# Optimization experiments

Measured on AMD Instinct MI355X. Metric: run time of the kernel, lower is better.

The kernel has to match this reference:

```python
import jax, jax.numpy as jnp
import numpy as np

B, N, NFEAT = 8, 5000, 15
NUM_CLASSES_IN = 12          # len(elem_labels)
D_IN = NUM_CLASSES_IN + NFEAT - 1  # 26
D_DIST = 256
D_HID = 256
BIN_SIZE = 100
NBINS = N // BIN_SIZE        # 50
K = 16                       # num_neighbors
DIST_MULT = 0.1
MAX_HALF_BINS = 100          # max_num_bins // 2
NUM_ID_OUT, NUM_REG_OUT = 8, 4


def _pairwise_dist(A):
    # A: [nbins, bs, d] -> [nbins, bs, bs]
    na = jnp.sum(A * A, -1)
    d2 = na[..., :, None] - 2.0 * jnp.einsum('...nd,...md->...nm', A, A) + na[..., None, :]
    return jnp.sqrt(jnp.maximum(d2, 1e-6))


def _build_edges(points, rot):
    # points: [N, D_DIST]; LSH binning then per-bin kNN (exp(-dist_mult * dist) affinities)
    mul = points @ rot[:, :NBINS // 2]
    cmul = jnp.concatenate([mul, -mul], axis=-1)
    bin_idx = jnp.argmax(cmul, axis=-1)
    bins_split = jnp.argsort(bin_idx).reshape(NBINS, BIN_SIZE)   # [nbins, bs] point ids
    parts = points[bins_split]                                   # [nbins, bs, d]
    dm = jnp.exp(-DIST_MULT * _pairwise_dist(parts))             # [nbins, bs, bs]
    vals, idx = jax.lax.top_k(dm, K)                             # [nbins, bs, K]
    dst = jax.vmap(lambda b, i: b[i])(bins_split, idx)           # global dst ids
    src = jnp.broadcast_to(bins_split[:, :, None], dst.shape)
    return src.reshape(-1), dst.reshape(-1), vals.reshape(-1)    # nnz = N*K


def _ghconv(x, src, dst, vals, theta, W_h, W_t, b_t):
    # x: [N, H]; edge list (src, dst, vals); duplicates sum, matching tf.sparse.add
    deg = jax.ops.segment_sum(vals, src, num_segments=N)
    norm = jnp.power(deg + 1e-6, -0.5)[:, None]
    f_hom = (x @ theta) * norm
    agg = jax.ops.segment_sum(vals[:, None] * f_hom[dst], src, num_segments=N) * norm
    f_het = x @ W_h
    gate = jax.nn.sigmoid(x @ W_t + b_t)
    return jax.nn.selu(gate * agg + (1.0 - gate) * f_het)


def setup_inputs() -> dict:
    key = jax.random.key(0)
    ks = jax.random.split(key, 32)
    w = lambda i, shape, s=0.02: (s * jax.random.normal(ks[i], shape)).astype(jnp.float32)
    ids = jax.random.randint(ks[0], (B, N, 1), 0, NUM_CLASSES_IN).astype(jnp.float32)
    props = jax.random.normal(ks[1], (B, N, NFEAT - 1), dtype=jnp.float32)
    X = jnp.concatenate([ids, props], axis=-1)
    return {
        'X': X,
        'rot': w(2, (D_DIST, MAX_HALF_BINS), 1.0),
        'W_emb': w(3, (D_IN, D_DIST)), 'b_emb': w(4, (D_DIST,)),
        'Wenc_id': w(5, (D_IN, D_HID)), 'benc_id': w(6, (D_HID,)),
        'theta_id': w(7, (D_HID, D_HID)), 'Wh_id': w(8, (D_HID, D_HID)),
        'Wt_id': w(9, (D_HID, D_HID)), 'bt_id': w(10, (D_HID,)),
        'Wdec_id': w(11, (D_HID, D_HID)), 'bdec_id': w(12, (D_HID,)),
        'Wout_id': w(13, (D_HID, NUM_ID_OUT)), 'bout_id': w(14, (NUM_ID_OUT,)),
        'Wenc_reg': w(15, (D_IN, D_HID)), 'benc_reg': w(16, (D_HID,)),
        'theta_reg': w(17, (D_HID, D_HID)), 'Wh_reg': w(18, (D_HID, D_HID)),
        'Wt_reg': w(19, (D_HID, D_HID)), 'bt_reg': w(20, (D_HID,)),
        'Wdec_reg': w(21, (D_HID, D_HID)), 'bdec_reg': w(22, (D_HID,)),
        'Wout_reg': w(23, (D_HID, NUM_REG_OUT)), 'bout_reg': w(24, (NUM_REG_OUT,)),
    }


def reference(X, rot, W_emb, b_emb,
              Wenc_id, benc_id, theta_id, Wh_id, Wt_id, bt_id, Wdec_id, bdec_id, Wout_id, bout_id,
              Wenc_reg, benc_reg, theta_reg, Wh_reg, Wt_reg, bt_reg, Wdec_reg, bdec_reg, Wout_reg, bout_reg):
    # InputEncoding: one-hot class id + remaining features
    enc = jnp.concatenate(
        [jax.nn.one_hot(X[:, :, 0].astype(jnp.int32), NUM_CLASSES_IN, dtype=jnp.float32),
         X[:, :, 1:]], axis=-1)                                  # [B, N, 26]
    emb = enc @ W_emb + b_emb                                     # distance embedding
    src, dst, vals = jax.vmap(_build_edges, in_axes=(0, None))(emb, rot)

    def branch(Wenc, benc, theta, Wh, Wt, bt, Wdec, bdec, Wout, bout):
        x = jax.nn.selu(enc @ Wenc + benc)
        x = jax.vmap(lambda xb, s, d, v: _ghconv(xb, s, d, v, theta, Wh, Wt, bt))(x, src, dst, vals)
        x = jax.nn.selu(x @ Wdec + bdec)
        return x @ Wout + bout

    out_id = branch(Wenc_id, benc_id, theta_id, Wh_id, Wt_id, bt_id, Wdec_id, bdec_id, Wout_id, bout_id)
    out_reg = branch(Wenc_reg, benc_reg, theta_reg, Wh_reg, Wt_reg, bt_reg, Wdec_reg, bdec_reg, Wout_reg, bout_reg)
    return out_id, out_reg
```

## Files before the change

### kernel.cpp

```cpp
#include <hip/hip_runtime.h>
#include <hip/hip_bf16.h>
#include <cstdint>
#include <cstddef>

#define NB     8
#define NLOC   5000
#define NPTS   40000
#define DIN    26
#define DH     256
#define NBINS  50
#define BSZ    100
#define KNN    16
#define KP     104

static const size_t OFF_BHI  = 40960000;
static const size_t OFF_BLO  = 41353216;
static const size_t OFF_BDHI = 41746432;
static const size_t OFF_BDLO = 41877504;
static const size_t OFF_ENC  = 81920000;
static const size_t OFF_BIN  = 86080000;
static const size_t OFF_ORD  = 86240000;
static const size_t OFF_NRM  = 86400000;
static const size_t OFF_EVAL = 86560000;
static const size_t OFF_EDST = 89120000;
static const size_t OFF_KEYS = 91680000;
static const size_t OFF_AXHI = 91680000;
static const size_t OFF_AXLO = 112160000;
static const size_t OFF_NA   = 132640000;
static const size_t OFF_FHET = 132640000;
static const size_t OFF_GATE = 173600000;

typedef __attribute__((ext_vector_type(8))) short short8;
typedef __attribute__((ext_vector_type(4))) float f32x4;

__device__ __forceinline__ float selu_f(float x) {
  const float scale = 1.0507009873554805f, alpha = 1.6732632423543772f;
  return x > 0.f ? scale * x : scale * alpha * expm1f(x);
}

__device__ __forceinline__ void split_bf16(float v, __hip_bfloat16& h, __hip_bfloat16& l) {
  h = __float2bfloat16(v);
  l = __float2bfloat16(v - __bfloat162float(h));
}

#define EPB 16
__global__ __launch_bounds__(256) void k_enc_emb(
    const float* __restrict__ X, const float* __restrict__ Wemb,
    const float* __restrict__ bemb, float* __restrict__ enc,
    double* __restrict__ emb) {
  __shared__ float xb[EPB * 15];
  const int tid = threadIdx.x;
  const int r0 = blockIdx.x * EPB;
  if (tid < EPB * 15) xb[tid] = X[(size_t)r0 * 15 + tid];
  double wcol[DIN];
  #pragma unroll
  for (int c = 0; c < DIN; c++) wcol[c] = (double)Wemb[c * DH + tid];
  const double bcol = (double)bemb[tid];
  __syncthreads();
  #pragma unroll 1
  for (int p = 0; p < EPB; p++) {
    const int id = (int)xb[p * 15];
    double acc = 0.0;
    #pragma unroll
    for (int c = 0; c < 12; c++)
      acc += ((c == id) ? 1.0 : 0.0) * wcol[c];
    #pragma unroll
    for (int c = 12; c < DIN; c++)
      acc += (double)xb[p * 15 + (c - 11)] * wcol[c];
    emb[(size_t)(r0 + p) * DH + tid] = acc + bcol;
  }
  #pragma unroll
  for (int t = 0; t < 2; t++) {
    int idx = t * 256 + tid;
    if (idx < EPB * DIN) {
      int p = idx / DIN, c = idx - p * DIN;
      int id = (int)xb[p * 15];
      float v = (c < 12) ? ((c == id) ? 1.f : 0.f) : xb[p * 15 + (c - 11)];
      enc[(size_t)(r0 + p) * DIN + c] = v;
    }
  }
}

#define MULPTS 16
__global__ __launch_bounds__(512) void k_mul(
    const double* __restrict__ emb, const float* __restrict__ rot,
    int* __restrict__ bin_idx) {
  __shared__ double ebuf[MULPTS][258];
  __shared__ float  rotT[25][257];
  __shared__ double mulb[MULPTS][26];
  const int tid = threadIdx.x;
  const int r0 = blockIdx.x * MULPTS;
  for (int idx = tid; idx < 25 * DH; idx += 512) {
    int d = idx / 25, j = idx - d * 25;
    rotT[j][d] = rot[d * 100 + j];
  }
  for (int idx = tid; idx < MULPTS * DH; idx += 512) {
    int p = idx >> 8, d = idx & 255;
    ebuf[p][d] = emb[(size_t)(r0 + p) * DH + d];
  }
  __syncthreads();
  if (tid < MULPTS * 25) {
    int p = tid / 25, j = tid - p * 25;
    double a = 0.0;
    #pragma unroll 4
    for (int d = 0; d < DH; d++) a += ebuf[p][d] * (double)rotT[j][d];
    mulb[p][j] = a;
  }
  __syncthreads();
  if (tid < MULPTS) {
    double best = -1e300; int bi = 0;
    #pragma unroll 1
    for (int jj = 0; jj < 2 * 25; jj++) {
      double v = (jj < 25) ? mulb[tid][jj] : -mulb[tid][jj - 25];
      if (v > best) { best = v; bi = jj; }
    }
    bin_idx[r0 + tid] = bi;
  }
}

#define SCH 20
__global__ __launch_bounds__(256) void k_sort(
    const int* __restrict__ bin_idx, int* __restrict__ order) {
  const int b = blockIdx.x;
  __shared__ unsigned short cnt[256][NBINS + 2];
  __shared__ int base[NBINS];
  __shared__ int bl[NLOC];
  const int tid = threadIdx.x;
  for (int j = 0; j < NBINS; j++) cnt[tid][j] = 0;
  for (int n = tid; n < NLOC; n += 256) bl[n] = bin_idx[b * NLOC + n];
  __syncthreads();
  const int s = tid * SCH;
  const int e = (s + SCH < NLOC) ? s + SCH : NLOC;
  for (int n = s; n < e; n++) cnt[tid][bl[n]]++;
  __syncthreads();
  if (tid < NBINS) {
    int run = 0;
    for (int t = 0; t < 256; t++) {
      int c = cnt[t][tid];
      cnt[t][tid] = (unsigned short)run;
      run += c;
    }
    base[tid] = run;
  }
  __syncthreads();
  if (tid == 0) {
    int r = 0;
    for (int j = 0; j < NBINS; j++) { int t = base[j]; base[j] = r; r += t; }
  }
  __syncthreads();
  for (int n = s; n < e; n++) {
    int j = bl[n];
    int pos = base[j] + cnt[tid][j];
    cnt[tid][j]++;
    order[b * NLOC + pos] = n;
  }
}

__global__ __launch_bounds__(256) void k_norm(
    const double* __restrict__ emb, const int* __restrict__ order,
    double* __restrict__ na) {
  const int s = blockIdx.x * 4 + (threadIdx.x >> 6);
  const int lane = threadIdx.x & 63;
  const int row = (s / NLOC) * NLOC + order[s];
  const double* p = &emb[(size_t)row * DH + lane * 4];
  double2 a = *(const double2*)p;
  double2 b = *(const double2*)(p + 2);
  double sum = a.x * a.x + a.y * a.y + b.x * b.x + b.y * b.y;
  #pragma unroll
  for (int off = 32; off >= 1; off >>= 1) sum += __shfl_xor(sum, off);
  if (lane == 0) na[s] = sum;
}

#define DQR 112
__global__ __launch_bounds__(256) void k_dist(
    const double* __restrict__ emb, const int* __restrict__ order,
    const double* __restrict__ na, double* __restrict__ keys) {
  __shared__ double P[DQR][34];
  __shared__ double naL[DQR];
  __shared__ int rid[DQR];
  const int bin = blockIdx.x;
  const int rh  = blockIdx.y;
  const int gb0 = bin * BSZ;
  const int brow = (bin / NBINS) * NLOC;
  const int tid = threadIdx.x;
  const int tx = tid & 15, ty = tid >> 4;
  if (tid < DQR) {
    int rr = tid < BSZ ? tid : BSZ - 1;
    rid[tid] = brow + order[gb0 + rr];
    naL[tid] = na[gb0 + rr];
  }
  __syncthreads();
  size_t srow[7];
  int scol[7], sr[7];
  #pragma unroll
  for (int q = 0; q < 7; q++) {
    int idx = q * 256 + tid;
    sr[q] = idx >> 4;
    scol[q] = (idx & 15) * 2;
    srow[q] = (size_t)rid[sr[q]] * DH;
  }
  int ar[4];
  #pragma unroll
  for (int i = 0; i < 4; i++) {
    int pr = rh * 50 + ty + 16 * i;
    ar[i] = pr < DQR ? pr : DQR - 1;
  }
  double acc[4][7] = {};
  double2 buf[7];
  #pragma unroll
  for (int q = 0; q < 7; q++)
    buf[q] = *(const double2*)&emb[srow[q] + scol[q]];
  for (int kc = 0; kc < 8; kc++) {
    __syncthreads();
    #pragma unroll
    for (int q = 0; q < 7; q++) {
      P[sr[q]][scol[q]]     = buf[q].x;
      P[sr[q]][scol[q] + 1] = buf[q].y;
    }
    __syncthreads();
    if (kc < 7) {
      #pragma unroll
      for (int q = 0; q < 7; q++)
        buf[q] = *(const double2*)&emb[srow[q] + (kc + 1) * 32 + scol[q]];
    }
    #pragma unroll 2
    for (int kk = 0; kk < 32; kk++) {
      double b[7];
      #pragma unroll
      for (int j = 0; j < 7; j++) b[j] = P[tx + 16 * j][kk];
      #pragma unroll
      for (int i = 0; i < 4; i++) {
        double a = P[ar[i]][kk];
        #pragma unroll
        for (int j = 0; j < 7; j++) acc[i][j] += a * b[j];
      }
    }
  }
  #pragma unroll
  for (int i = 0; i < 4; i++) {
    int lr = ty + 16 * i;
    if (lr >= 50) continue;
    int gi = rh * 50 + lr;
    #pragma unroll
    for (int j = 0; j < 7; j++) {
      int gj = tx + 16 * j;
      if (gj >= BSZ) continue;
      double t = naL[gi] - 2.0 * acc[i][j];
      t += naL[gj];
      keys[(size_t)(gb0 + gi) * KP + gj] = (t > 1e-6) ? t : 1e-6;
    }
  }
}

__global__ __launch_bounds__(256) void k_topk(
    const double* __restrict__ keys, float* __restrict__ evals,
    int* __restrict__ edstl, float* __restrict__ normv) {
  const int g = threadIdx.x >> 4;
  const int l = threadIdx.x & 15;
  const int row = blockIdx.x * 16 + g;
  const unsigned long long* kr =
      (const unsigned long long*)(keys + (size_t)row * KP);
  unsigned long long c[7];
  #pragma unroll
  for (int s = 0; s < 7; s++) {
    int j = s * 16 + l;
    c[s] = (j < BSZ) ? kr[j] : ~0ull;
  }
  float deg = 0.f, myev = 0.f;
  int myidx = 0;
  #pragma unroll 1
  for (int k = 0; k < KNN; k++) {
    unsigned long long mv = c[0];
    int ms = 0;
    #pragma unroll
    for (int s = 1; s < 7; s++)
      if (c[s] < mv) { mv = c[s]; ms = s; }
    int idx = ms * 16 + l;
    #pragma unroll
    for (int off = 8; off >= 1; off >>= 1) {
      unsigned long long ov = __shfl_xor(mv, off);
      int oi = __shfl_xor(idx, off);
      if (ov < mv || (ov == mv && oi < idx)) { mv = ov; idx = oi; }
    }
    float ev = expf(-0.1f * sqrtf((float)__longlong_as_double(mv)));
    deg += ev;
    if (l == k) { myev = ev; myidx = idx; }
    const int own = idx & 15, slot = idx >> 4;
    if (l == own) {
      #pragma unroll
      for (int s = 0; s < 7; s++)
        if (slot == s) c[s] = ~0ull;
    }
  }
  evals[(size_t)row * KNN + l] = myev;
  edstl[(size_t)row * KNN + l] = myidx;
  if (l == 0) normv[row] = 1.f / sqrtf(deg + 1e-6f);
}

__global__ __launch_bounds__(256) void k_encmm(
    const float* __restrict__ enc, const float* __restrict__ W,
    const float* __restrict__ bias, __hip_bfloat16* __restrict__ hi,
    __hip_bfloat16* __restrict__ lo) {
  const int r = blockIdx.x;
  __shared__ float e[DIN];
  const int tid = threadIdx.x;
  if (tid < DIN) e[tid] = enc[(size_t)r * DIN + tid];
  __syncthreads();
  float acc = 0.f;
  #pragma unroll 1
  for (int c = 0; c < DIN; c++) acc += e[c] * W[c * DH + tid];
  float v = selu_f(acc + bias[tid]);
  __hip_bfloat16 h, l;
  split_bf16(v, h, l);
  hi[(size_t)r * DH + tid] = h;
  lo[(size_t)r * DH + tid] = l;
}

__global__ __launch_bounds__(256) void k_cvt_w4(
    const float* __restrict__ W0, const float* __restrict__ W1,
    const float* __restrict__ W2, const float* __restrict__ W3,
    __hip_bfloat16* __restrict__ Bhi, __hip_bfloat16* __restrict__ Blo,
    __hip_bfloat16* __restrict__ Bdhi, __hip_bfloat16* __restrict__ Bdlo) {
  __shared__ float t[32][33];
  const int z = blockIdx.z;
  const float* W = (z == 0) ? W0 : (z == 1) ? W1 : (z == 2) ? W2 : W3;
  __hip_bfloat16* hi = (z < 3) ? Bhi + (size_t)z * 65536 : Bdhi;
  __hip_bfloat16* lo = (z < 3) ? Blo + (size_t)z * 65536 : Bdlo;
  const int tid = threadIdx.x, tx = tid & 31, ty = tid >> 5;
  const int k0 = blockIdx.x * 32, n0 = blockIdx.y * 32;
  #pragma unroll
  for (int r = 0; r < 4; r++)
    t[ty + r * 8][tx] = W[(size_t)(k0 + ty + r * 8) * 256 + n0 + tx];
  __syncthreads();
  #pragma unroll
  for (int r = 0; r < 4; r++) {
    int n = ty + r * 8;
    float v = t[tx][n];
    __hip_bfloat16 h, l;
    split_bf16(v, h, l);
    hi[(size_t)(n0 + n) * 256 + k0 + tx] = h;
    lo[(size_t)(n0 + n) * 256 + k0 + tx] = l;
  }
}

#define MF_SMEM (4 * 128 * 40 * 2)
template <int MODE>
__global__ __launch_bounds__(256, 4) void k_mfma(
    const ushort* __restrict__ Ahi, const ushort* __restrict__ Alo,
    const ushort* __restrict__ Bhi, const ushort* __restrict__ Blo,
    const float* __restrict__ bias,
    float* __restrict__ O0, float* __restrict__ O1, float* __restrict__ O2) {
  extern __shared__ char mfs[];
  short* As0 = (short*)mfs;
  short* As1 = As0 + 128 * 40;
  short* Bs0 = As1 + 128 * 40;
  short* Bs1 = Bs0 + 128 * 40;
  const int NX = (MODE == 0) ? 6 : 2;
  const int total = NX * 313;
  const int q = total >> 3, rr8 = total & 7;
  const int xcd = blockIdx.x & 7, pos = blockIdx.x >> 3;
  const int lw = (xcd < rr8 ? xcd * (q + 1) : rr8 * (q + 1) + (xcd - rr8) * q) + pos;
  const int m0 = (lw / NX) * 128;
  const int nx = lw - (lw / NX) * NX;
  const int n0 = nx * 128;
  const int tid = threadIdx.x;
  const int lane = tid & 63, wid = tid >> 6;
  const int wr = wid >> 1, wc = wid & 1;
  const int lm = lane & 15, lg = lane >> 4;
  f32x4 acc[4][4];
  #pragma unroll
  for (int i = 0; i < 4; i++)
    #pragma unroll
    for (int j = 0; j < 4; j++)
      #pragma unroll
      for (int r = 0; r < 4; r++) acc[i][j][r] = 0.f;

  for (int k0 = 0; k0 < 256; k0 += 32) {
    #pragma unroll
    for (int it = 0; it < 2; it++) {
      int idx = it * 256 + tid;
      int r = idx >> 2, c = (idx & 3) * 8;
      int gm = m0 + r; if (gm >= NPTS) gm = NPTS - 1;
      *(uint4*)&As0[r * 40 + c] = *(const uint4*)&Ahi[(size_t)gm * 256 + k0 + c];
      *(uint4*)&As1[r * 40 + c] = *(const uint4*)&Alo[(size_t)gm * 256 + k0 + c];
      *(uint4*)&Bs0[r * 40 + c] = *(const uint4*)&Bhi[(size_t)(n0 + r) * 256 + k0 + c];
      *(uint4*)&Bs1[r * 40 + c] = *(const uint4*)&Blo[(size_t)(n0 + r) * 256 + k0 + c];
    }
    __syncthreads();
    const int lk = lg * 8;
    short8 aH[4], bH[4], aL[4], bL[4];
    #pragma unroll
    for (int mf = 0; mf < 4; mf++)
      aH[mf] = *(const short8*)&As0[(wr * 64 + mf * 16 + lm) * 40 + lk];
    #pragma unroll
    for (int nf = 0; nf < 4; nf++)
      bH[nf] = *(const short8*)&Bs0[(wc * 64 + nf * 16 + lm) * 40 + lk];
    #pragma unroll
    for (int mf = 0; mf < 4; mf++)
      #pragma unroll
      for (int nf = 0; nf < 4; nf++)
        acc[mf][nf] = __builtin_amdgcn_mfma_f32_16x16x32_bf16(aH[mf], bH[nf], acc[mf][nf], 0, 0, 0);
    #pragma unroll
    for (int nf = 0; nf < 4; nf++)
      bL[nf] = *(const short8*)&Bs1[(wc * 64 + nf * 16 + lm) * 40 + lk];
    #pragma unroll
    for (int mf = 0; mf < 4; mf++)
      #pragma unroll
      for (int nf = 0; nf < 4; nf++)
        acc[mf][nf] = __builtin_amdgcn_mfma_f32_16x16x32_bf16(aH[mf], bL[nf], acc[mf][nf], 0, 0, 0);
    #pragma unroll
    for (int mf = 0; mf < 4; mf++)
      aL[mf] = *(const short8*)&As1[(wr * 64 + mf * 16 + lm) * 40 + lk];
    #pragma unroll
    for (int mf = 0; mf < 4; mf++)
      #pragma unroll
      for (int nf = 0; nf < 4; nf++)
        acc[mf][nf] = __builtin_amdgcn_mfma_f32_16x16x32_bf16(aL[mf], bH[nf], acc[mf][nf], 0, 0, 0);
    __syncthreads();
  }

  float* Out; int cb;
  if (MODE == 0) {
    const int seg = nx >> 1;
    Out = (seg == 0) ? O0 : ((seg == 1) ? O1 : O2);
    cb = (nx & 1) * 128;
  } else {
    Out = O0; cb = n0;
  }
  const bool do_gate = (MODE == 0) && (nx >> 1) == 2;
  #pragma unroll
  for (int mf = 0; mf < 4; mf++) {
    const int gm0 = m0 + wr * 64 + mf * 16 + lg * 4;
    #pragma unroll
    for (int nf = 0; nf < 4; nf++) {
      const int gn = cb + wc * 64 + nf * 16 + lm;
      #pragma unroll
      for (int r = 0; r < 4; r++) {
        const int gm = gm0 + r;
        if (gm >= NPTS) continue;
        float c = acc[mf][nf][r];
        if (MODE == 1)      c = selu_f(c + bias[gn]);
        else if (do_gate)   c = 1.f / (1.f + expf(-(c + bias[gn])));
        Out[(size_t)gm * 256 + gn] = c;
      }
    }
  }
}

#define GAT_SMEM (100 * 256 * 4 + 1600 * 8 + 100 * 4 + 100 * 4)
__global__ __launch_bounds__(1024) void k_gatherb(
    const float* __restrict__ hth, const float* __restrict__ fhet,
    const float* __restrict__ gate, const float* __restrict__ evals,
    const int* __restrict__ edstl, const int* __restrict__ order,
    const float* __restrict__ normv, __hip_bfloat16* __restrict__ yhi,
    __hip_bfloat16* __restrict__ ylo) {
  extern __shared__ char gsm[];
  float*  hl  = (float*)gsm;
  float2* cwL = (float2*)(gsm + 102400);
  int*    idsL = (int*)(gsm + 102400 + 12800);
  float*  nvL  = (float*)(gsm + 102400 + 12800 + 400);
  const int bin = blockIdx.x;
  const int gb0 = bin * 100;
  const int brow = (bin / NBINS) * NLOC;
  const int tid = threadIdx.x;
  const int p = tid >> 8, d = tid & 255;
  if (tid < BSZ) {
    idsL[tid] = order[gb0 + tid];
    nvL[tid] = normv[gb0 + tid];
  }
  __syncthreads();
  for (int t = tid; t < BSZ * KNN; t += 1024) {
    int lj = edstl[(size_t)gb0 * KNN + t];
    cwL[t] = make_float2(evals[(size_t)gb0 * KNN + t] * nvL[lj],
                         __int_as_float(lj));
  }
  for (int idx = tid; idx < BSZ * DH; idx += 1024) {
    int i = idx >> 8, dd = idx & 255;
    hl[i * 256 + dd] = hth[(size_t)(brow + idsL[i]) * DH + dd];
  }
  __syncthreads();
  size_t srow_n = (size_t)(brow + idsL[p]) * DH;
  float g_n = gate[srow_n + d], fh_n = fhet[srow_n + d];
  #pragma unroll 1
  for (int ii = 0; ii < 25; ii++) {
    const int i = ii * 4 + p;
    const size_t srow = srow_n;
    const float g = g_n, fh = fh_n;
    if (ii < 24) {
      srow_n = (size_t)(brow + idsL[i + 4]) * DH;
      g_n = gate[srow_n + d];
      fh_n = fhet[srow_n + d];
    }
    float acc = 0.f;
    #pragma unroll
    for (int k = 0; k < KNN; k++) {
      float2 cw = cwL[i * KNN + k];
      acc += cw.x * hl[__float_as_int(cw.y) * 256 + d];
    }
    float v = selu_f(g * (nvL[i] * acc) + (1.f - g) * fh);
    __hip_bfloat16 h, l;
    split_bf16(v, h, l);
    yhi[srow + d] = h;
    ylo[srow + d] = l;
  }
}

template <int OW>
__global__ __launch_bounds__(256) void k_out(
    const float* __restrict__ Z, const float* __restrict__ W,
    const float* __restrict__ bias, float* __restrict__ out) {
  const int p0 = blockIdx.x * 32;
  __shared__ float zb[32][257];
  const int tid = threadIdx.x;
  for (int idx = tid; idx < 32 * DH; idx += 256) {
    int p = idx >> 8, d = idx & 255;
    zb[p][d] = Z[(size_t)(p0 + p) * DH + d];
  }
  __syncthreads();
  if (tid < 32 * OW) {
    int p = tid / OW, o = tid - (tid / OW) * OW;
    float acc = 0.f;
    #pragma unroll 4
    for (int d = 0; d < DH; d++) acc += zb[p][d] * W[d * OW + o];
    out[(size_t)(p0 + p) * OW + o] = acc + bias[o];
  }
}

extern "C" void kernel_launch(void* const* d_in, const int* in_sizes, int n_in,
                              void* d_out, int out_size, void* d_ws, size_t ws_size,
                              hipStream_t stream) {
  const float* X     = (const float*)d_in[0];
  const float* rot   = (const float*)d_in[1];
  const float* W_emb = (const float*)d_in[2];
  const float* b_emb = (const float*)d_in[3];
  const float* Wenc[2]  = {(const float*)d_in[4],  (const float*)d_in[14]};
  const float* benc[2]  = {(const float*)d_in[5],  (const float*)d_in[15]};
  const float* theta[2] = {(const float*)d_in[6],  (const float*)d_in[16]};
  const float* Wh[2]    = {(const float*)d_in[7],  (const float*)d_in[17]};
  const float* Wt[2]    = {(const float*)d_in[8],  (const float*)d_in[18]};
  const float* bt[2]    = {(const float*)d_in[9],  (const float*)d_in[19]};
  const float* Wdec[2]  = {(const float*)d_in[10], (const float*)d_in[20]};
  const float* bdec[2]  = {(const float*)d_in[11], (const float*)d_in[21]};
  const float* Wout[2]  = {(const float*)d_in[12], (const float*)d_in[22]};
  const float* bout[2]  = {(const float*)d_in[13], (const float*)d_in[23]};

  char* w = (char*)d_ws;
  double* emb   = (double*)(w + 0);
  float*  hth   = (float*)(w + 0);
  __hip_bfloat16* Bhi  = (__hip_bfloat16*)(w + OFF_BHI);
  __hip_bfloat16* Blo  = (__hip_bfloat16*)(w + OFF_BLO);
  __hip_bfloat16* Bdhi = (__hip_bfloat16*)(w + OFF_BDHI);
  __hip_bfloat16* Bdlo = (__hip_bfloat16*)(w + OFF_BDLO);
  float*  enc   = (float*)(w + OFF_ENC);
  int*    binid = (int*)(w + OFF_BIN);
  int*    order = (int*)(w + OFF_ORD);
  float*  normv = (float*)(w + OFF_NRM);
  float*  evals = (float*)(w + OFF_EVAL);
  int*    edstl = (int*)(w + OFF_EDST);
  double* keys  = (double*)(w + OFF_KEYS);
  double* na    = (double*)(w + OFF_NA);
  __hip_bfloat16* Axhi = (__hip_bfloat16*)(w + OFF_AXHI);
  __hip_bfloat16* Axlo = (__hip_bfloat16*)(w + OFF_AXLO);
  float*  fhet  = (float*)(w + OFF_FHET);
  float*  gate  = (float*)(w + OFF_GATE);
  float*  zbuf  = (float*)(w + OFF_GATE);
  float*  outp  = (float*)d_out;

  (void)hipFuncSetAttribute(reinterpret_cast<const void*>(k_gatherb),
                            hipFuncAttributeMaxDynamicSharedMemorySize, GAT_SMEM);
  (void)hipFuncSetAttribute(reinterpret_cast<const void*>(k_mfma<0>),
                            hipFuncAttributeMaxDynamicSharedMemorySize, MF_SMEM);
  (void)hipFuncSetAttribute(reinterpret_cast<const void*>(k_mfma<1>),
                            hipFuncAttributeMaxDynamicSharedMemorySize, MF_SMEM);

  k_enc_emb<<<NPTS / EPB, 256, 0, stream>>>(X, W_emb, b_emb, enc, emb);
  k_mul<<<NPTS / MULPTS, 512, 0, stream>>>(emb, rot, binid);
  k_sort<<<NB, 256, 0, stream>>>(binid, order);
  k_norm<<<NPTS / 4, 256, 0, stream>>>(emb, order, na);
  k_dist<<<dim3(NB * NBINS, 2), 256, 0, stream>>>(emb, order, na, keys);
  k_topk<<<NPTS / 16, 256, 0, stream>>>(keys, evals, edstl, normv);

  const dim3 gw(8, 8, 4);
  for (int br = 0; br < 2; br++) {
    k_cvt_w4<<<gw, 256, 0, stream>>>(theta[br], Wh[br], Wt[br], Wdec[br],
                                     Bhi, Blo, Bdhi, Bdlo);
    k_encmm<<<NPTS, 256, 0, stream>>>(enc, Wenc[br], benc[br], Axhi, Axlo);
    k_mfma<0><<<6 * 313, 256, MF_SMEM, stream>>>((const ushort*)Axhi, (const ushort*)Axlo,
                                                 (const ushort*)Bhi, (const ushort*)Blo,
                                                 bt[br], hth, fhet, gate);
    k_gatherb<<<NB * NBINS, 1024, GAT_SMEM, stream>>>(hth, fhet, gate, evals, edstl,
                                                      order, normv, Axhi, Axlo);
    k_mfma<1><<<2 * 313, 256, MF_SMEM, stream>>>((const ushort*)Axhi, (const ushort*)Axlo,
                                                 (const ushort*)Bdhi, (const ushort*)Bdlo,
                                                 bdec[br], zbuf, nullptr, nullptr);
    if (br == 0) k_out<8><<<NPTS / 32, 256, 0, stream>>>(zbuf, Wout[0], bout[0], outp);
    else         k_out<4><<<NPTS / 32, 256, 0, stream>>>(zbuf, Wout[1], bout[1], outp + (size_t)NPTS * 8);
  }
}
```

Measured before the change: 776.5 us.

## Fuse norm into embedding kernel and top-k selection into distance kernel

Squared row norms are now computed inside the embedding kernel with a wave reduction, indexed by unsorted point id, which removes the separate norm kernel and its re-read of the embedding. The top-k selection now runs directly on the distance accumulators held in registers inside the distance kernel, so the double-precision key matrix is never written to or read back from global memory. This removes two launches and a round trip of intermediate data. In exchange, the distance kernel's register pressure and tail work grow, which could lower its occupancy.

```diff
diff --git a/kernel.cpp b/kernel.cpp
--- a/kernel.cpp
+++ b/kernel.cpp
@@ -11,7 +11,6 @@
 #define NBINS  50
 #define BSZ    100
 #define KNN    16
-#define KP     104
 
 static const size_t OFF_BHI  = 40960000;
 static const size_t OFF_BLO  = 41353216;
@@ -23,7 +22,6 @@
 static const size_t OFF_NRM  = 86400000;
 static const size_t OFF_EVAL = 86560000;
 static const size_t OFF_EDST = 89120000;
-static const size_t OFF_KEYS = 91680000;
 static const size_t OFF_AXHI = 91680000;
 static const size_t OFF_AXLO = 112160000;
 static const size_t OFF_NA   = 132640000;
@@ -47,9 +45,11 @@
 __global__ __launch_bounds__(256) void k_enc_emb(
     const float* __restrict__ X, const float* __restrict__ Wemb,
     const float* __restrict__ bemb, float* __restrict__ enc,
-    double* __restrict__ emb) {
+    double* __restrict__ emb, double* __restrict__ na_u) {
   __shared__ float xb[EPB * 15];
-  const int tid = threadIdx.x;
+  __shared__ double partd[EPB][4];
+  const int tid = threadIdx.x;
+  const int lane = tid & 63, wid = tid >> 6;
   const int r0 = blockIdx.x * EPB;
   if (tid < EPB * 15) xb[tid] = X[(size_t)r0 * 15 + tid];
   double wcol[DIN];
@@ -67,8 +67,16 @@
     #pragma unroll
     for (int c = 12; c < DIN; c++)
       acc += (double)xb[p * 15 + (c - 11)] * wcol[c];
-    emb[(size_t)(r0 + p) * DH + tid] = acc + bcol;
-  }
+    const double v = acc + bcol;
+    emb[(size_t)(r0 + p) * DH + tid] = v;
+    double sq = v * v;
+    #pragma unroll
+    for (int off = 32; off >= 1; off >>= 1) sq += __shfl_xor(sq, off);
+    if (lane == 0) partd[p][wid] = sq;
+  }
+  __syncthreads();
+  if (tid < EPB)
+    na_u[r0 + tid] = partd[tid][0] + partd[tid][1] + partd[tid][2] + partd[tid][3];
   #pragma unroll
   for (int t = 0; t < 2; t++) {
     int idx = t * 256 + tid;
@@ -156,25 +164,11 @@
   }
 }
 
-__global__ __launch_bounds__(256) void k_norm(
-    const double* __restrict__ emb, const int* __restrict__ order,
-    double* __restrict__ na) {
-  const int s = blockIdx.x * 4 + (threadIdx.x >> 6);
-  const int lane = threadIdx.x & 63;
-  const int row = (s / NLOC) * NLOC + order[s];
-  const double* p = &emb[(size_t)row * DH + lane * 4];
-  double2 a = *(const double2*)p;
-  double2 b = *(const double2*)(p + 2);
-  double sum = a.x * a.x + a.y * a.y + b.x * b.x + b.y * b.y;
-  #pragma unroll
-  for (int off = 32; off >= 1; off >>= 1) sum += __shfl_xor(sum, off);
-  if (lane == 0) na[s] = sum;
-}
-
 #define DQR 112
 __global__ __launch_bounds__(256) void k_dist(
     const double* __restrict__ emb, const int* __restrict__ order,
-    const double* __restrict__ na, double* __restrict__ keys) {
+    const double* __restrict__ na_u, float* __restrict__ evals,
+    int* __restrict__ edstl, float* __restrict__ normv) {
   __shared__ double P[DQR][34];
   __shared__ double naL[DQR];
   __shared__ int rid[DQR];
@@ -186,8 +180,9 @@
   const int tx = tid & 15, ty = tid >> 4;
   if (tid < DQR) {
     int rr = tid < BSZ ? tid : BSZ - 1;
-    rid[tid] = brow + order[gb0 + rr];
-    naL[tid] = na[gb0 + rr];
+    int g = brow + order[gb0 + rr];
+    rid[tid] = g;
+    naL[tid] = na_u[g];
   }
   __syncthreads();
   size_t srow[7];
@@ -236,65 +231,55 @@
       }
     }
   }
-  #pragma unroll
+  const int l = tx;
+  #pragma unroll 1
   for (int i = 0; i < 4; i++) {
-    int lr = ty + 16 * i;
+    const int lr = ty + 16 * i;
     if (lr >= 50) continue;
-    int gi = rh * 50 + lr;
+    const int gi = rh * 50 + lr;
+    const double nai = naL[gi];
+    unsigned long long c[7];
     #pragma unroll
     for (int j = 0; j < 7; j++) {
       int gj = tx + 16 * j;
-      if (gj >= BSZ) continue;
-      double t = naL[gi] - 2.0 * acc[i][j];
-      t += naL[gj];
-      keys[(size_t)(gb0 + gi) * KP + gj] = (t > 1e-6) ? t : 1e-6;
-    }
-  }
-}
-
-__global__ __launch_bounds__(256) void k_topk(
-    const double* __restrict__ keys, float* __restrict__ evals,
-    int* __restrict__ edstl, float* __restrict__ normv) {
-  const int g = threadIdx.x >> 4;
-  const int l = threadIdx.x & 15;
-  const int row = blockIdx.x * 16 + g;
-  const unsigned long long* kr =
-      (const unsigned long long*)(keys + (size_t)row * KP);
-  unsigned long long c[7];
-  #pragma unroll
-  for (int s = 0; s < 7; s++) {
-    int j = s * 16 + l;
-    c[s] = (j < BSZ) ? kr[j] : ~0ull;
-  }
-  float deg = 0.f, myev = 0.f;
-  int myidx = 0;
-  #pragma unroll 1
-  for (int k = 0; k < KNN; k++) {
-    unsigned long long mv = c[0];
-    int ms = 0;
-    #pragma unroll
-    for (int s = 1; s < 7; s++)
-      if (c[s] < mv) { mv = c[s]; ms = s; }
-    int idx = ms * 16 + l;
-    #pragma unroll
-    for (int off = 8; off >= 1; off >>= 1) {
-      unsigned long long ov = __shfl_xor(mv, off);
-      int oi = __shfl_xor(idx, off);
-      if (ov < mv || (ov == mv && oi < idx)) { mv = ov; idx = oi; }
-    }
-    float ev = expf(-0.1f * sqrtf((float)__longlong_as_double(mv)));
-    deg += ev;
-    if (l == k) { myev = ev; myidx = idx; }
-    const int own = idx & 15, slot = idx >> 4;
-    if (l == own) {
-      #pragma unroll
-      for (int s = 0; s < 7; s++)
-        if (slot == s) c[s] = ~0ull;
-    }
-  }
-  evals[(size_t)row * KNN + l] = myev;
-  edstl[(size_t)row * KNN + l] = myidx;
-  if (l == 0) normv[row] = 1.f / sqrtf(deg + 1e-6f);
+      if (gj < BSZ) {
+        double t = nai - 2.0 * acc[i][j];
+        t += naL[gj];
+        c[j] = __double_as_longlong((t > 1e-6) ? t : 1e-6);
+      } else {
+        c[j] = ~0ull;
+      }
+    }
+    float deg = 0.f, myev = 0.f;
+    int myidx = 0;
+    #pragma unroll 1
+    for (int k = 0; k < KNN; k++) {
+      unsigned long long mv = c[0];
+      int ms = 0;
+      #pragma unroll
+      for (int s = 1; s < 7; s++)
+        if (c[s] < mv) { mv = c[s]; ms = s; }
+      int idx = ms * 16 + l;
+      #pragma unroll
+      for (int off = 8; off >= 1; off >>= 1) {
+        unsigned long long ov = __shfl_xor(mv, off);
+        int oi = __shfl_xor(idx, off);
+        if (ov < mv || (ov == mv && oi < idx)) { mv = ov; idx = oi; }
+      }
+      float ev = expf(-0.1f * sqrtf((float)__longlong_as_double(mv)));
+      deg += ev;
+      if (l == k) { myev = ev; myidx = idx; }
+      const int own = idx & 15, slot = idx >> 4;
+      if (l == own) {
+        #pragma unroll
+        for (int s = 0; s < 7; s++)
+          if (slot == s) c[s] = ~0ull;
+      }
+    }
+    evals[(size_t)(gb0 + gi) * KNN + l] = myev;
+    edstl[(size_t)(gb0 + gi) * KNN + l] = myidx;
+    if (l == 0) normv[gb0 + gi] = 1.f / sqrtf(deg + 1e-6f);
+  }
 }
 
 __global__ __launch_bounds__(256) void k_encmm(
@@ -557,8 +542,7 @@
   float*  normv = (float*)(w + OFF_NRM);
   float*  evals = (float*)(w + OFF_EVAL);
   int*    edstl = (int*)(w + OFF_EDST);
-  double* keys  = (double*)(w + OFF_KEYS);
-  double* na    = (double*)(w + OFF_NA);
+  double* na_u  = (double*)(w + OFF_NA);
   __hip_bfloat16* Axhi = (__hip_bfloat16*)(w + OFF_AXHI);
   __hip_bfloat16* Axlo = (__hip_bfloat16*)(w + OFF_AXLO);
   float*  fhet  = (float*)(w + OFF_FHET);
@@ -573,12 +557,10 @@
   (void)hipFuncSetAttribute(reinterpret_cast<const void*>(k_mfma<1>),
                             hipFuncAttributeMaxDynamicSharedMemorySize, MF_SMEM);
 
-  k_enc_emb<<<NPTS / EPB, 256, 0, stream>>>(X, W_emb, b_emb, enc, emb);
+  k_enc_emb<<<NPTS / EPB, 256, 0, stream>>>(X, W_emb, b_emb, enc, emb, na_u);
   k_mul<<<NPTS / MULPTS, 512, 0, stream>>>(emb, rot, binid);
   k_sort<<<NB, 256, 0, stream>>>(binid, order);
-  k_norm<<<NPTS / 4, 256, 0, stream>>>(emb, order, na);
-  k_dist<<<dim3(NB * NBINS, 2), 256, 0, stream>>>(emb, order, na, keys);
-  k_topk<<<NPTS / 16, 256, 0, stream>>>(keys, evals, edstl, normv);
+  k_dist<<<dim3(NB * NBINS, 2), 256, 0, stream>>>(emb, order, na_u, evals, edstl, normv);
 
   const dim3 gw(8, 8, 4);
   for (int br = 0; br < 2; br++) {
```

New measurement: 874.7 us. +12.7%, slower.
